# Optimization experiments

Hardware: AMD Instinct MI355X
Metric: run time of the kernel (lower is better)

The kernel has to match this reference:

```python
import jax, jax.numpy as jnp
import numpy as np

D_MODEL = 768
NUM_HEADS = 12
HEAD_DIM = D_MODEL // NUM_HEADS
THETA = 10000.0
SEQ = 4096
BATCH = 2


def setup_inputs() -> dict:
    key = jax.random.key(0)
    ks = jax.random.split(key, 5)
    std = np.sqrt(2.0 / (D_MODEL + D_MODEL)).astype(np.float32)
    x = jax.random.normal(ks[0], (BATCH, SEQ, D_MODEL), dtype=jnp.float32)
    token_positions = jnp.arange(SEQ, dtype=jnp.int32)
    # Linear stores weight as (d_out, d_in), applied as x @ W.T
    wq = jax.random.normal(ks[1], (D_MODEL, D_MODEL), dtype=jnp.float32) * std
    wk = jax.random.normal(ks[2], (D_MODEL, D_MODEL), dtype=jnp.float32) * std
    wv = jax.random.normal(ks[3], (D_MODEL, D_MODEL), dtype=jnp.float32) * std
    wo = jax.random.normal(ks[4], (D_MODEL, D_MODEL), dtype=jnp.float32) * std
    return {"x": x, "token_positions": token_positions,
            "wq": wq, "wk": wk, "wv": wv, "wo": wo}


def _apply_rope(t, positions):
    # t: [B, H, S, hd], positions: [S]
    half = HEAD_DIM // 2
    inv_freq = THETA ** (-jnp.arange(0, HEAD_DIM, 2, dtype=jnp.float32) / HEAD_DIM)  # [half]
    angles = positions.astype(jnp.float32)[:, None] * inv_freq  # [S, half]
    cos = jnp.repeat(jnp.cos(angles), 2, axis=-1)  # [S, hd]
    sin = jnp.repeat(jnp.sin(angles), 2, axis=-1)  # [S, hd]
    # rotate pairs: (-x1, x0, -x3, x2, ...)
    t2 = jnp.stack([-t[..., 1::2], t[..., ::2]], axis=-1).reshape(t.shape)
    return t * cos + t2 * sin


def reference(x, token_positions, wq, wk, wv, wo):
    B, S, D = x.shape
    H, hd = NUM_HEADS, HEAD_DIM
    q = (x @ wq.T).reshape(B, S, H, hd).transpose(0, 2, 1, 3)  # [B,H,S,hd]
    k = (x @ wk.T).reshape(B, S, H, hd).transpose(0, 2, 1, 3)
    v = (x @ wv.T).reshape(B, S, H, hd).transpose(0, 2, 1, 3)
    q = _apply_rope(q, token_positions)
    k = _apply_rope(k, token_positions)
    scale = hd ** -0.5
    scores = jnp.einsum('bhqd,bhkd->bhqk', q, k) * scale  # [B,H,S,S]
    causal = jnp.tril(jnp.ones((S, S), dtype=bool))
    scores = jnp.where(causal, scores, -jnp.inf)
    att = jax.nn.softmax(scores, axis=-1)
    out = jnp.einsum('bhqk,bhkd->bhqd', att, v)  # [B,H,S,hd]
    out = out.transpose(0, 2, 1, 3).reshape(B, S, D)
    return out @ wo.T
```

## Files before the change

kernel.cpp:

```cpp
#include <hip/hip_runtime.h>
#include <hip/hip_bf16.h>
#include <stdint.h>

#define D_MODEL 768
#define NHEADS 12
#define HD 64
#define SEQ 4096
#define BATCH 2
#define MTOT (BATCH*SEQ)
#define BHN (BATCH*NHEADS)

typedef __attribute__((ext_vector_type(8))) short short8;
typedef __attribute__((ext_vector_type(4))) float f32x4;
typedef __attribute__((ext_vector_type(16))) float f32x16;
typedef __attribute__((ext_vector_type(4))) int i32x4;

__device__ inline unsigned short f2bf(float f) {
  union { float f; unsigned u; } v; v.f = f;
  unsigned r = (v.u + 0x7FFFu + ((v.u >> 16) & 1u)) >> 16;
  return (unsigned short)r;
}
__device__ inline unsigned cvtpk_bf16(float lo, float hi) {
  unsigned r;
  asm("v_cvt_pk_bf16_f32 %0, %1, %2" : "=v"(r) : "v"(lo), "v"(hi));
  return r;
}
__device__ inline void perm32swap(unsigned &a, unsigned &b) {
  asm("v_permlane32_swap_b32 %0, %1" : "+v"(a), "+v"(b));
}
__device__ inline float exp2fast(float x) {
  float r;
  asm("v_exp_f32 %0, %1" : "=v"(r) : "v"(x));
  return r;
}
__device__ inline void gload16(const void* g, void* l) {
  __builtin_amdgcn_global_load_lds(
      (const __attribute__((address_space(1))) unsigned int*)g,
      (__attribute__((address_space(3))) unsigned int*)l, 16, 0, 0);
}

__global__ void k_conv(const float* __restrict__ x,  const float* __restrict__ wq,
                       const float* __restrict__ wk, const float* __restrict__ wv,
                       const float* __restrict__ wo,
                       unsigned short* __restrict__ xb,  unsigned short* __restrict__ wqb,
                       unsigned short* __restrict__ wkb, unsigned short* __restrict__ wvb,
                       unsigned short* __restrict__ wob)
{
  int i = blockIdx.x * blockDim.x + threadIdx.x;
  const int X4 = MTOT*D_MODEL/4;
  const int W4 = D_MODEL*D_MODEL/4;
  const float* src; unsigned short* dst; int idx;
  if (i < X4) { src = x; dst = xb; idx = i; }
  else {
    int j = i - X4;
    if      (j <   W4) { src = wq; dst = wqb; idx = j; }
    else if (j < 2*W4) { src = wk; dst = wkb; idx = j -   W4; }
    else if (j < 3*W4) { src = wv; dst = wvb; idx = j - 2*W4; }
    else if (j < 4*W4) { src = wo; dst = wob; idx = j - 3*W4; }
    else return;
  }
  float4 v = ((const float4*)src)[idx];
  ushort4 o;
  o.x = f2bf(v.x); o.y = f2bf(v.y); o.z = f2bf(v.z); o.w = f2bf(v.w);
  ((ushort4*)dst)[idx] = o;
}

__global__ void k_ropetab(const int* __restrict__ pos, float* __restrict__ ct, float* __restrict__ st) {
  int i = blockIdx.x * blockDim.x + threadIdx.x;
  if (i >= SEQ*32) return;
  int s = i >> 5, j = i & 31;
  float p = (float)pos[s];
  const float L = 0.2878231366242557f;
  float freq = __expf(-L * (float)j);
  float a = p * freq;
  ct[i] = cosf(a);
  st[i] = sinf(a);
}

__global__ __launch_bounds__(256)
void k_gemm_qkv(const unsigned short* __restrict__ X,
                const unsigned short* __restrict__ Wq,
                const unsigned short* __restrict__ Wk,
                const unsigned short* __restrict__ Wv,
                unsigned short* __restrict__ Qp,
                unsigned short* __restrict__ Kp,
                unsigned short* __restrict__ VT,
                const float* __restrict__ ct,
                const float* __restrict__ st)
{
  __shared__ __align__(16) unsigned short As[2][128*32];
  __shared__ __align__(16) unsigned short Bs[2][128*32];
  const int tid = threadIdx.x;
  const int wave = tid >> 6, lane = tid & 63;
  const int lr = lane & 15, lg = lane >> 4;
  const int wr = wave >> 1, wc = wave & 1;
  const int m0 = blockIdx.x * 128;
  const int n0 = blockIdx.y * 128;
  const int z  = blockIdx.z;
  const unsigned short* B = (z == 0) ? Wq : (z == 1) ? Wk : Wv;
  const int K = 768;

  f32x4 acc[4][4] = {};
  const int srow = tid >> 2, scol = (tid & 3) << 3;
  const unsigned short* ag = X + (size_t)(m0 + srow) * K + scol;
  const unsigned short* bg = B + (size_t)(n0 + srow) * K + scol;

  {
    char* a0 = (char*)As[0] + wave*1024;
    char* a1 = (char*)As[0] + 4096 + wave*1024;
    char* b0 = (char*)Bs[0] + wave*1024;
    char* b1 = (char*)Bs[0] + 4096 + wave*1024;
    gload16(ag, a0);
    gload16(ag + (size_t)64*K, a1);
    gload16(bg, b0);
    gload16(bg + (size_t)64*K, b1);
  }
  int cur = 0;
  for (int k0 = 0; k0 < K; k0 += 32) {
    __syncthreads();
    if (k0 + 32 < K) {
      char* a0 = (char*)As[cur^1] + wave*1024;
      char* a1 = (char*)As[cur^1] + 4096 + wave*1024;
      char* b0 = (char*)Bs[cur^1] + wave*1024;
      char* b1 = (char*)Bs[cur^1] + 4096 + wave*1024;
      gload16(ag + k0 + 32, a0);
      gload16(ag + (size_t)64*K + k0 + 32, a1);
      gload16(bg + k0 + 32, b0);
      gload16(bg + (size_t)64*K + k0 + 32, b1);
    }
    short8 af[4], bfr[4];
    #pragma unroll
    for (int i = 0; i < 4; ++i)
      af[i] = *(const short8*)&As[cur][(wr*64 + i*16 + lr)*32 + lg*8];
    #pragma unroll
    for (int j = 0; j < 4; ++j)
      bfr[j] = *(const short8*)&Bs[cur][(wc*64 + j*16 + lr)*32 + lg*8];
    #pragma unroll
    for (int i = 0; i < 4; ++i)
      #pragma unroll
      for (int j = 0; j < 4; ++j)
        acc[i][j] = __builtin_amdgcn_mfma_f32_16x16x32_bf16(af[i], bfr[j], acc[i][j], 0, 0, 0);
    cur ^= 1;
  }

  #pragma unroll
  for (int i = 0; i < 4; ++i)
    #pragma unroll
    for (int j = 0; j < 4; ++j) {
      const int n = n0 + wc*64 + j*16 + lr;
      const int h = n >> 6, d = n & (HD-1);
      if (z == 2) {
        #pragma unroll
        for (int r = 0; r < 4; ++r) {
          int m = m0 + wr*64 + i*16 + lg*4 + r;
          int bb = m >> 12, s = m & (SEQ-1);
          VT[(((size_t)bb*NHEADS + h)*HD + d)*SEQ + s] = f2bf(acc[i][j][r]);
        }
      } else {
        unsigned short* dst = (z == 0) ? Qp : Kp;
        const float* cb = ct + (d >> 1);
        const float* sb = st + (d >> 1);
        #pragma unroll
        for (int r = 0; r < 4; ++r) {
          int m = m0 + wr*64 + i*16 + lg*4 + r;
          int bb = m >> 12, s = m & (SEQ-1);
          float vv = acc[i][j][r];
          float pp = __shfl_xor(vv, 1);
          float cs = cb[s << 5], sn = sb[s << 5];
          float res = (d & 1) ? (vv*cs + pp*sn) : (vv*cs - pp*sn);
          if (z == 0) res *= 0.18033688011112043f;
          dst[(((size_t)bb*NHEADS + h)*SEQ + s)*HD + d] = f2bf(res);
        }
      }
    }
}

__global__ __launch_bounds__(256)
void k_gemm_wo(const unsigned short* __restrict__ X,
               const unsigned short* __restrict__ W,
               float* __restrict__ out)
{
  __shared__ __align__(16) unsigned short As[2][128*32];
  __shared__ __align__(16) unsigned short Bs[2][128*32];
  const int tid = threadIdx.x;
  const int wave = tid >> 6, lane = tid & 63;
  const int lr = lane & 15, lg = lane >> 4;
  const int wr = wave >> 1, wc = wave & 1;
  const int m0 = blockIdx.x * 128;
  const int n0 = blockIdx.y * 128;
  const int K = 768;

  f32x4 acc[4][4] = {};
  const int srow = tid >> 2, scol = (tid & 3) << 3;
  const unsigned short* ag = X + (size_t)(m0 + srow) * K + scol;
  const unsigned short* bg = W + (size_t)(n0 + srow) * K + scol;

  {
    char* a0 = (char*)As[0] + wave*1024;
    char* a1 = (char*)As[0] + 4096 + wave*1024;
    char* b0 = (char*)Bs[0] + wave*1024;
    char* b1 = (char*)Bs[0] + 4096 + wave*1024;
    gload16(ag, a0);
    gload16(ag + (size_t)64*K, a1);
    gload16(bg, b0);
    gload16(bg + (size_t)64*K, b1);
  }
  int cur = 0;
  for (int k0 = 0; k0 < K; k0 += 32) {
    __syncthreads();
    if (k0 + 32 < K) {
      char* a0 = (char*)As[cur^1] + wave*1024;
      char* a1 = (char*)As[cur^1] + 4096 + wave*1024;
      char* b0 = (char*)Bs[cur^1] + wave*1024;
      char* b1 = (char*)Bs[cur^1] + 4096 + wave*1024;
      gload16(ag + k0 + 32, a0);
      gload16(ag + (size_t)64*K + k0 + 32, a1);
      gload16(bg + k0 + 32, b0);
      gload16(bg + (size_t)64*K + k0 + 32, b1);
    }
    short8 af[4], bfr[4];
    #pragma unroll
    for (int i = 0; i < 4; ++i)
      af[i] = *(const short8*)&As[cur][(wr*64 + i*16 + lr)*32 + lg*8];
    #pragma unroll
    for (int j = 0; j < 4; ++j)
      bfr[j] = *(const short8*)&Bs[cur][(wc*64 + j*16 + lr)*32 + lg*8];
    #pragma unroll
    for (int i = 0; i < 4; ++i)
      #pragma unroll
      for (int j = 0; j < 4; ++j)
        acc[i][j] = __builtin_amdgcn_mfma_f32_16x16x32_bf16(af[i], bfr[j], acc[i][j], 0, 0, 0);
    cur ^= 1;
  }

  #pragma unroll
  for (int i = 0; i < 4; ++i)
    #pragma unroll
    for (int j = 0; j < 4; ++j)
      #pragma unroll
      for (int r = 0; r < 4; ++r) {
        int m = m0 + wr*64 + i*16 + lg*4 + r;
        int n = n0 + wc*64 + j*16 + lr;
        out[(size_t)m*D_MODEL + n] = acc[i][j][r];
      }
}

__global__ __launch_bounds__(256, 3)
void k_attn(const unsigned short* __restrict__ Qp,
            const unsigned short* __restrict__ Kp,
            const unsigned short* __restrict__ VT,
            unsigned short* __restrict__ AO)
{
  __shared__ __align__(16) unsigned short Ks[2][64*64];
  __shared__ __align__(16) unsigned short Vs[2][64*64];

  const int tid = threadIdx.x;
  const int wave = tid >> 6, lane = tid & 63;
  const int qcol = lane & 31, hi = lane >> 5;

  const int u = blockIdx.x;
  const int kk = u >> 8, g = u & 255;
  const int rank = (kk == 0) ? g : (kk == 1) ? (767 - g) : (256 + g);
  const int cpair = rank / 24;
  const int bh = rank - cpair * 24;

  const int b = bh / NHEADS, h = bh % NHEADS;
  const int chunk = (wave < 2) ? cpair : 63 - cpair;
  const int qw = chunk * 64 + (wave & 1) * 32;
  const int nt = 64 - cpair;
  const int myNt = qw / 64 + 1;

  const unsigned short* Qh = Qp + (size_t)bh * SEQ * HD;
  const unsigned short* Kh = Kp + (size_t)bh * SEQ * HD;
  const unsigned short* Vh = VT + (size_t)bh * HD * SEQ;

  short8 qf[4];
  #pragma unroll
  for (int ds = 0; ds < 4; ++ds)
    qf[ds] = *(const short8*)(Qh + (size_t)(qw + qcol)*HD + ds*16 + hi*8);

  f32x16 o[2] = {};
  f32x16 lv = {};

  const int g_row = tid >> 3;
  const int sgp = ((tid & 7) ^ (g_row & 7)) * 8;

  {
    char* kb0 = (char*)Ks[0] + wave*1024;
    char* kb1 = (char*)Ks[0] + 4096 + wave*1024;
    char* vb0 = (char*)Vs[0] + wave*1024;
    char* vb1 = (char*)Vs[0] + 4096 + wave*1024;
    gload16(Kh + (size_t)g_row*HD + sgp, kb0);
    gload16(Kh + (size_t)(g_row + 32)*HD + sgp, kb1);
    gload16(Vh + (size_t)g_row*SEQ + sgp, vb0);
    gload16(Vh + (size_t)(g_row + 32)*SEQ + sgp, vb1);
  }
  __syncthreads();

  int cur = 0;
  for (int kt = 0; kt < nt; ++kt) {
    if (kt + 1 < nt) {
      const size_t kb = (size_t)(kt + 1) * 64;
      char* kb0 = (char*)Ks[cur^1] + wave*1024;
      char* kb1 = (char*)Ks[cur^1] + 4096 + wave*1024;
      char* vb0 = (char*)Vs[cur^1] + wave*1024;
      char* vb1 = (char*)Vs[cur^1] + 4096 + wave*1024;
      gload16(Kh + (kb + g_row)*HD + sgp, kb0);
      gload16(Kh + (kb + g_row + 32)*HD + sgp, kb1);
      gload16(Vh + (size_t)g_row*SEQ + kb + sgp, vb0);
      gload16(Vh + (size_t)(g_row + 32)*SEQ + kb + sgp, vb1);
    }
    if (kt < myNt) {
      const char* Kb = (const char*)Ks[cur];
      const char* Vb = (const char*)Vs[cur];
      f32x16 c[2];
      __builtin_amdgcn_s_setprio(1);
      #pragma unroll
      for (int kc = 0; kc < 2; ++kc) {
        f32x16 acc = {};
        #pragma unroll
        for (int ds = 0; ds < 4; ++ds) {
          const int row = kc*32 + qcol;
          short8 kf = *(const short8*)(Kb + row*128 + ((ds*32 + hi*16) ^ ((row & 7) << 4)));
          acc = __builtin_amdgcn_mfma_f32_32x32x16_bf16(kf, qf[ds], acc, 0, 0, 0);
        }
        c[kc] = acc;
      }
      __builtin_amdgcn_s_setprio(0);
      if (kt == myNt - 1) {
        const int q = qw + qcol;
        #pragma unroll
        for (int kc = 0; kc < 2; ++kc)
          #pragma unroll
          for (int r = 0; r < 16; ++r) {
            int key = kt*64 + kc*32 + (r & 3) + 8*(r >> 2) + 4*hi;
            if (key > q) c[kc][r] = -1e30f;
          }
      }
      #pragma unroll
      for (int kc = 0; kc < 2; ++kc)
        #pragma unroll
        for (int r = 0; r < 16; ++r)
          c[kc][r] = exp2fast(c[kc][r]);
      #pragma unroll
      for (int r = 0; r < 16; ++r) lv[r] += c[0][r] + c[1][r];
      unsigned U[8][2];
      #pragma unroll
      for (int g2 = 0; g2 < 8; ++g2) {
        const int fc = g2 >> 2, gq = g2 & 3;
        U[g2][0] = cvtpk_bf16(c[fc][4*gq + 0], c[fc][4*gq + 1]);
        U[g2][1] = cvtpk_bf16(c[fc][4*gq + 2], c[fc][4*gq + 3]);
      }
      #pragma unroll
      for (int ks = 0; ks < 4; ++ks) {
        unsigned j0 = U[2*ks][0], j2 = U[2*ks+1][0];
        perm32swap(j0, j2);
        unsigned j1 = U[2*ks][1], j3 = U[2*ks+1][1];
        perm32swap(j1, j3);
        union { unsigned u[4]; short8 s; } pf;
        pf.u[0] = j0; pf.u[1] = j1; pf.u[2] = j2; pf.u[3] = j3;
        __builtin_amdgcn_s_setprio(1);
        #pragma unroll
        for (int dc = 0; dc < 2; ++dc) {
          const int row = dc*32 + qcol;
          short8 vf = *(const short8*)(Vb + row*128 + ((ks*32 + hi*16) ^ ((row & 7) << 4)));
          o[dc] = __builtin_amdgcn_mfma_f32_32x32x16_bf16(vf, pf.s, o[dc], 0, 0, 0);
        }
        __builtin_amdgcn_s_setprio(0);
      }
    }
    __syncthreads();
    cur ^= 1;
  }

  float s0 = (lv[0]+lv[1]) + (lv[2]+lv[3]);
  float s1 = (lv[4]+lv[5]) + (lv[6]+lv[7]);
  float s2 = (lv[8]+lv[9]) + (lv[10]+lv[11]);
  float s3 = (lv[12]+lv[13]) + (lv[14]+lv[15]);
  float ssum = (s0+s1) + (s2+s3);
  ssum += __shfl_xor(ssum, 32);
  const float inv = 1.0f / ssum;
  const size_t rowbase = ((size_t)b*SEQ + qw + qcol) * D_MODEL + h*HD;
  #pragma unroll
  for (int dc = 0; dc < 2; ++dc)
    #pragma unroll
    for (int g2 = 0; g2 < 4; ++g2) {
      ushort4 pk;
      pk.x = f2bf(o[dc][4*g2 + 0] * inv);
      pk.y = f2bf(o[dc][4*g2 + 1] * inv);
      pk.z = f2bf(o[dc][4*g2 + 2] * inv);
      pk.w = f2bf(o[dc][4*g2 + 3] * inv);
      const int d0 = dc*32 + 8*g2 + 4*hi;
      *(ushort4*)(AO + rowbase + d0) = pk;
    }
}

extern "C" void kernel_launch(void* const* d_in, const int* in_sizes, int n_in,
                              void* d_out, int out_size, void* d_ws, size_t ws_size,
                              hipStream_t stream)
{
  const float* x  = (const float*)d_in[0];
  const int* posi = (const int*)d_in[1];
  const float* wq = (const float*)d_in[2];
  const float* wk = (const float*)d_in[3];
  const float* wv = (const float*)d_in[4];
  const float* wo = (const float*)d_in[5];
  float* out = (float*)d_out;

  char* ws = (char*)d_ws;
  size_t off = 0;
  auto alloc = [&](size_t bytes) {
    char* p = ws + off;
    off += (bytes + 255) & ~(size_t)255;
    return p;
  };
  unsigned short* xb  = (unsigned short*)alloc((size_t)MTOT*D_MODEL*2);
  unsigned short* wqb = (unsigned short*)alloc((size_t)D_MODEL*D_MODEL*2);
  unsigned short* wkb = (unsigned short*)alloc((size_t)D_MODEL*D_MODEL*2);
  unsigned short* wvb = (unsigned short*)alloc((size_t)D_MODEL*D_MODEL*2);
  unsigned short* wob = (unsigned short*)alloc((size_t)D_MODEL*D_MODEL*2);
  unsigned short* Qb  = (unsigned short*)alloc((size_t)BHN*SEQ*HD*2);
  unsigned short* Kb  = (unsigned short*)alloc((size_t)BHN*SEQ*HD*2);
  unsigned short* VTb = (unsigned short*)alloc((size_t)BHN*HD*SEQ*2);
  unsigned short* AOb = (unsigned short*)alloc((size_t)MTOT*D_MODEL*2);
  float* ct = (float*)alloc((size_t)SEQ*32*4);
  float* st = (float*)alloc((size_t)SEQ*32*4);

  const int total4 = MTOT*D_MODEL/4 + 4*(D_MODEL*D_MODEL/4);
  k_conv<<<(total4 + 255)/256, 256, 0, stream>>>(x, wq, wk, wv, wo, xb, wqb, wkb, wvb, wob);
  k_ropetab<<<(SEQ*32 + 255)/256, 256, 0, stream>>>(posi, ct, st);

  k_gemm_qkv<<<dim3(MTOT/128, D_MODEL/128, 3), 256, 0, stream>>>(xb, wqb, wkb, wvb, Qb, Kb, VTb, ct, st);
  k_attn<<<dim3(768), 256, 0, stream>>>(Qb, Kb, VTb, AOb);
  k_gemm_wo<<<dim3(MTOT/128, D_MODEL/128), 256, 0, stream>>>(AOb, wob, out);
}
```

Measured before the change: 167.4 us.

## Triple-buffer attention K/V tiles and software-pipeline QK^T ahead of softmax

The attention kernel moves from two shared-memory K/V buffers to three, prefetching two tiles ahead, and computes the QK^T MFMAs for the next tile while the current tile's exp and PV work is still in flight. The loop is unrolled by two so the score registers can ping-pong. The RoPE cos/sin table is also transposed to [freq][seq], so the QKV epilogue can load four consecutive positions as one vector. The costs are more LDS per block, which may reduce occupancy under launch_bounds(256,3), and higher register pressure from holding two score tiles at once.

```diff
diff --git a/kernel.cpp b/kernel.cpp
--- a/kernel.cpp
+++ b/kernel.cpp
@@ -68,7 +68,7 @@
 __global__ void k_ropetab(const int* __restrict__ pos, float* __restrict__ ct, float* __restrict__ st) {
   int i = blockIdx.x * blockDim.x + threadIdx.x;
   if (i >= SEQ*32) return;
-  int s = i >> 5, j = i & 31;
+  int s = i & (SEQ-1), j = i >> 12;
   float p = (float)pos[s];
   const float L = 0.2878231366242557f;
   float freq = __expf(-L * (float)j);
@@ -158,18 +158,19 @@
         }
       } else {
         unsigned short* dst = (z == 0) ? Qp : Kp;
-        const float* cb = ct + (d >> 1);
-        const float* sb = st + (d >> 1);
+        const int jrow = d >> 1;
+        const int mb = m0 + wr*64 + i*16 + lg*4;
+        const int bb = mb >> 12;
+        const int sbase = mb & (SEQ-1);
+        f32x4 cs4 = *(const f32x4*)(ct + (size_t)jrow*SEQ + sbase);
+        f32x4 sn4 = *(const f32x4*)(st + (size_t)jrow*SEQ + sbase);
         #pragma unroll
         for (int r = 0; r < 4; ++r) {
-          int m = m0 + wr*64 + i*16 + lg*4 + r;
-          int bb = m >> 12, s = m & (SEQ-1);
           float vv = acc[i][j][r];
           float pp = __shfl_xor(vv, 1);
-          float cs = cb[s << 5], sn = sb[s << 5];
-          float res = (d & 1) ? (vv*cs + pp*sn) : (vv*cs - pp*sn);
+          float res = (d & 1) ? (vv*cs4[r] + pp*sn4[r]) : (vv*cs4[r] - pp*sn4[r]);
           if (z == 0) res *= 0.18033688011112043f;
-          dst[(((size_t)bb*NHEADS + h)*SEQ + s)*HD + d] = f2bf(res);
+          dst[(((size_t)bb*NHEADS + h)*SEQ + (sbase + r))*HD + d] = f2bf(res);
         }
       }
     }
@@ -251,8 +252,8 @@
             const unsigned short* __restrict__ VT,
             unsigned short* __restrict__ AO)
 {
-  __shared__ __align__(16) unsigned short Ks[2][64*64];
-  __shared__ __align__(16) unsigned short Vs[2][64*64];
+  __shared__ __align__(16) unsigned short Ks[3][64*64];
+  __shared__ __align__(16) unsigned short Vs[3][64*64];
 
   const int tid = threadIdx.x;
   const int wave = tid >> 6, lane = tid & 63;
@@ -285,48 +286,40 @@
   const int g_row = tid >> 3;
   const int sgp = ((tid & 7) ^ (g_row & 7)) * 8;
 
-  {
-    char* kb0 = (char*)Ks[0] + wave*1024;
-    char* kb1 = (char*)Ks[0] + 4096 + wave*1024;
-    char* vb0 = (char*)Vs[0] + wave*1024;
-    char* vb1 = (char*)Vs[0] + 4096 + wave*1024;
-    gload16(Kh + (size_t)g_row*HD + sgp, kb0);
-    gload16(Kh + (size_t)(g_row + 32)*HD + sgp, kb1);
-    gload16(Vh + (size_t)g_row*SEQ + sgp, vb0);
-    gload16(Vh + (size_t)(g_row + 32)*SEQ + sgp, vb1);
-  }
+  auto STAGE = [&](int t, int bi) {
+    const size_t kb = (size_t)t * 64;
+    gload16(Kh + (kb + g_row)*HD + sgp,        (char*)Ks[bi] + wave*1024);
+    gload16(Kh + (kb + g_row + 32)*HD + sgp,   (char*)Ks[bi] + 4096 + wave*1024);
+    gload16(Vh + (size_t)g_row*SEQ + kb + sgp,      (char*)Vs[bi] + wave*1024);
+    gload16(Vh + (size_t)(g_row + 32)*SEQ + kb + sgp, (char*)Vs[bi] + 4096 + wave*1024);
+  };
+  auto QKT = [&](int bi, f32x16 (&cc)[2]) {
+    const char* Kb = (const char*)Ks[bi];
+    __builtin_amdgcn_s_setprio(1);
+    #pragma unroll
+    for (int kc = 0; kc < 2; ++kc) {
+      f32x16 acc = {};
+      #pragma unroll
+      for (int ds = 0; ds < 4; ++ds) {
+        const int row = kc*32 + qcol;
+        short8 kf = *(const short8*)(Kb + row*128 + ((ds*32 + hi*16) ^ ((row & 7) << 4)));
+        acc = __builtin_amdgcn_mfma_f32_32x32x16_bf16(kf, qf[ds], acc, 0, 0, 0);
+      }
+      cc[kc] = acc;
+    }
+    __builtin_amdgcn_s_setprio(0);
+  };
+
+  STAGE(0, 0);
+  if (nt > 1) STAGE(1, 1);
   __syncthreads();
-
-  int cur = 0;
-  for (int kt = 0; kt < nt; ++kt) {
-    if (kt + 1 < nt) {
-      const size_t kb = (size_t)(kt + 1) * 64;
-      char* kb0 = (char*)Ks[cur^1] + wave*1024;
-      char* kb1 = (char*)Ks[cur^1] + 4096 + wave*1024;
-      char* vb0 = (char*)Vs[cur^1] + wave*1024;
-      char* vb1 = (char*)Vs[cur^1] + 4096 + wave*1024;
-      gload16(Kh + (kb + g_row)*HD + sgp, kb0);
-      gload16(Kh + (kb + g_row + 32)*HD + sgp, kb1);
-      gload16(Vh + (size_t)g_row*SEQ + kb + sgp, vb0);
-      gload16(Vh + (size_t)(g_row + 32)*SEQ + kb + sgp, vb1);
-    }
+  f32x16 cA[2], cB[2];
+  QKT(0, cA);
+
+  int kt = 0, bc = 0, bn = 1, bs = 2;
+  auto ITER = [&](f32x16 (&ccur)[2], f32x16 (&cnxt)[2]) {
+    if (kt + 2 < nt) STAGE(kt + 2, bs);
     if (kt < myNt) {
-      const char* Kb = (const char*)Ks[cur];
-      const char* Vb = (const char*)Vs[cur];
-      f32x16 c[2];
-      __builtin_amdgcn_s_setprio(1);
-      #pragma unroll
-      for (int kc = 0; kc < 2; ++kc) {
-        f32x16 acc = {};
-        #pragma unroll
-        for (int ds = 0; ds < 4; ++ds) {
-          const int row = kc*32 + qcol;
-          short8 kf = *(const short8*)(Kb + row*128 + ((ds*32 + hi*16) ^ ((row & 7) << 4)));
-          acc = __builtin_amdgcn_mfma_f32_32x32x16_bf16(kf, qf[ds], acc, 0, 0, 0);
-        }
-        c[kc] = acc;
-      }
-      __builtin_amdgcn_s_setprio(0);
       if (kt == myNt - 1) {
         const int q = qw + qcol;
         #pragma unroll
@@ -334,23 +327,25 @@
           #pragma unroll
           for (int r = 0; r < 16; ++r) {
             int key = kt*64 + kc*32 + (r & 3) + 8*(r >> 2) + 4*hi;
-            if (key > q) c[kc][r] = -1e30f;
+            if (key > q) ccur[kc][r] = -1e30f;
           }
       }
       #pragma unroll
       for (int kc = 0; kc < 2; ++kc)
         #pragma unroll
         for (int r = 0; r < 16; ++r)
-          c[kc][r] = exp2fast(c[kc][r]);
-      #pragma unroll
-      for (int r = 0; r < 16; ++r) lv[r] += c[0][r] + c[1][r];
+          ccur[kc][r] = exp2fast(ccur[kc][r]);
+      #pragma unroll
+      for (int r = 0; r < 16; ++r) lv[r] += ccur[0][r] + ccur[1][r];
+      if (kt + 1 < myNt) QKT(bn, cnxt);
       unsigned U[8][2];
       #pragma unroll
       for (int g2 = 0; g2 < 8; ++g2) {
         const int fc = g2 >> 2, gq = g2 & 3;
-        U[g2][0] = cvtpk_bf16(c[fc][4*gq + 0], c[fc][4*gq + 1]);
-        U[g2][1] = cvtpk_bf16(c[fc][4*gq + 2], c[fc][4*gq + 3]);
-      }
+        U[g2][0] = cvtpk_bf16(ccur[fc][4*gq + 0], ccur[fc][4*gq + 1]);
+        U[g2][1] = cvtpk_bf16(ccur[fc][4*gq + 2], ccur[fc][4*gq + 3]);
+      }
+      const char* Vb = (const char*)Vs[bc];
       #pragma unroll
       for (int ks = 0; ks < 4; ++ks) {
         unsigned j0 = U[2*ks][0], j2 = U[2*ks+1][0];
@@ -370,8 +365,12 @@
       }
     }
     __syncthreads();
-    cur ^= 1;
-  }
+    const int t = bc; bc = bn; bn = bs; bs = t;
+    ++kt;
+  };
+
+  while (kt + 1 < nt) { ITER(cA, cB); ITER(cB, cA); }
+  if (kt < nt) ITER(cA, cB);
 
   float s0 = (lv[0]+lv[1]) + (lv[2]+lv[3]);
   float s1 = (lv[4]+lv[5]) + (lv[6]+lv[7]);
```

Result: slower. 180.1 us (+7.6%).

## Transpose RoPE table for vector loads; compute softmax row sums via MFMA

Applied to the files above, without the earlier changes.

The RoPE cos/sin tables are now stored frequency-major, so the QK GEMM epilogue reads four consecutive positions with one vector load instead of four strided scalar loads. In the attention kernel, the per-row sum of exponentials is now produced by an extra MFMA against a vector of bf16 ones. This replaces the 32 VALU adds per tile and the final cross-lane reduction. The sum is now taken over the bf16-rounded probabilities, which matches what multiplies V, at the cost of one extra MFMA per k-step.

```diff
diff --git a/kernel.cpp b/kernel.cpp
--- a/kernel.cpp
+++ b/kernel.cpp
@@ -68,7 +68,7 @@
 __global__ void k_ropetab(const int* __restrict__ pos, float* __restrict__ ct, float* __restrict__ st) {
   int i = blockIdx.x * blockDim.x + threadIdx.x;
   if (i >= SEQ*32) return;
-  int s = i >> 5, j = i & 31;
+  int s = i & (SEQ-1), j = i >> 12;
   float p = (float)pos[s];
   const float L = 0.2878231366242557f;
   float freq = __expf(-L * (float)j);
@@ -158,18 +158,19 @@
         }
       } else {
         unsigned short* dst = (z == 0) ? Qp : Kp;
-        const float* cb = ct + (d >> 1);
-        const float* sb = st + (d >> 1);
+        const int jrow = d >> 1;
+        const int mb = m0 + wr*64 + i*16 + lg*4;
+        const int bb = mb >> 12;
+        const int sbase = mb & (SEQ-1);
+        f32x4 cs4 = *(const f32x4*)(ct + (size_t)jrow*SEQ + sbase);
+        f32x4 sn4 = *(const f32x4*)(st + (size_t)jrow*SEQ + sbase);
         #pragma unroll
         for (int r = 0; r < 4; ++r) {
-          int m = m0 + wr*64 + i*16 + lg*4 + r;
-          int bb = m >> 12, s = m & (SEQ-1);
           float vv = acc[i][j][r];
           float pp = __shfl_xor(vv, 1);
-          float cs = cb[s << 5], sn = sb[s << 5];
-          float res = (d & 1) ? (vv*cs + pp*sn) : (vv*cs - pp*sn);
+          float res = (d & 1) ? (vv*cs4[r] + pp*sn4[r]) : (vv*cs4[r] - pp*sn4[r]);
           if (z == 0) res *= 0.18033688011112043f;
-          dst[(((size_t)bb*NHEADS + h)*SEQ + s)*HD + d] = f2bf(res);
+          dst[(((size_t)bb*NHEADS + h)*SEQ + (sbase + r))*HD + d] = f2bf(res);
         }
       }
     }
@@ -279,21 +280,21 @@
   for (int ds = 0; ds < 4; ++ds)
     qf[ds] = *(const short8*)(Qh + (size_t)(qw + qcol)*HD + ds*16 + hi*8);
 
+  short8 onesf;
+  #pragma unroll
+  for (int i = 0; i < 8; ++i) onesf[i] = (short)0x3F80;
+
   f32x16 o[2] = {};
-  f32x16 lv = {};
+  f32x16 lacc = {};
 
   const int g_row = tid >> 3;
   const int sgp = ((tid & 7) ^ (g_row & 7)) * 8;
 
   {
-    char* kb0 = (char*)Ks[0] + wave*1024;
-    char* kb1 = (char*)Ks[0] + 4096 + wave*1024;
-    char* vb0 = (char*)Vs[0] + wave*1024;
-    char* vb1 = (char*)Vs[0] + 4096 + wave*1024;
-    gload16(Kh + (size_t)g_row*HD + sgp, kb0);
-    gload16(Kh + (size_t)(g_row + 32)*HD + sgp, kb1);
-    gload16(Vh + (size_t)g_row*SEQ + sgp, vb0);
-    gload16(Vh + (size_t)(g_row + 32)*SEQ + sgp, vb1);
+    gload16(Kh + (size_t)g_row*HD + sgp,          (char*)Ks[0] + wave*1024);
+    gload16(Kh + (size_t)(g_row + 32)*HD + sgp,   (char*)Ks[0] + 4096 + wave*1024);
+    gload16(Vh + (size_t)g_row*SEQ + sgp,         (char*)Vs[0] + wave*1024);
+    gload16(Vh + (size_t)(g_row + 32)*SEQ + sgp,  (char*)Vs[0] + 4096 + wave*1024);
   }
   __syncthreads();
 
@@ -301,14 +302,10 @@
   for (int kt = 0; kt < nt; ++kt) {
     if (kt + 1 < nt) {
       const size_t kb = (size_t)(kt + 1) * 64;
-      char* kb0 = (char*)Ks[cur^1] + wave*1024;
-      char* kb1 = (char*)Ks[cur^1] + 4096 + wave*1024;
-      char* vb0 = (char*)Vs[cur^1] + wave*1024;
-      char* vb1 = (char*)Vs[cur^1] + 4096 + wave*1024;
-      gload16(Kh + (kb + g_row)*HD + sgp, kb0);
-      gload16(Kh + (kb + g_row + 32)*HD + sgp, kb1);
-      gload16(Vh + (size_t)g_row*SEQ + kb + sgp, vb0);
-      gload16(Vh + (size_t)(g_row + 32)*SEQ + kb + sgp, vb1);
+      gload16(Kh + (kb + g_row)*HD + sgp,            (char*)Ks[cur^1] + wave*1024);
+      gload16(Kh + (kb + g_row + 32)*HD + sgp,       (char*)Ks[cur^1] + 4096 + wave*1024);
+      gload16(Vh + (size_t)g_row*SEQ + kb + sgp,     (char*)Vs[cur^1] + wave*1024);
+      gload16(Vh + (size_t)(g_row + 32)*SEQ + kb + sgp, (char*)Vs[cur^1] + 4096 + wave*1024);
     }
     if (kt < myNt) {
       const char* Kb = (const char*)Ks[cur];
@@ -342,8 +339,6 @@
         #pragma unroll
         for (int r = 0; r < 16; ++r)
           c[kc][r] = exp2fast(c[kc][r]);
-      #pragma unroll
-      for (int r = 0; r < 16; ++r) lv[r] += c[0][r] + c[1][r];
       unsigned U[8][2];
       #pragma unroll
       for (int g2 = 0; g2 < 8; ++g2) {
@@ -366,6 +361,7 @@
           short8 vf = *(const short8*)(Vb + row*128 + ((ks*32 + hi*16) ^ ((row & 7) << 4)));
           o[dc] = __builtin_amdgcn_mfma_f32_32x32x16_bf16(vf, pf.s, o[dc], 0, 0, 0);
         }
+        lacc = __builtin_amdgcn_mfma_f32_32x32x16_bf16(onesf, pf.s, lacc, 0, 0, 0);
         __builtin_amdgcn_s_setprio(0);
       }
     }
@@ -373,13 +369,7 @@
     cur ^= 1;
   }
 
-  float s0 = (lv[0]+lv[1]) + (lv[2]+lv[3]);
-  float s1 = (lv[4]+lv[5]) + (lv[6]+lv[7]);
-  float s2 = (lv[8]+lv[9]) + (lv[10]+lv[11]);
-  float s3 = (lv[12]+lv[13]) + (lv[14]+lv[15]);
-  float ssum = (s0+s1) + (s2+s3);
-  ssum += __shfl_xor(ssum, 32);
-  const float inv = 1.0f / ssum;
+  const float inv = 1.0f / lacc[0];
   const size_t rowbase = ((size_t)b*SEQ + qw + qcol) * D_MODEL + h*HD;
   #pragma unroll
   for (int dc = 0; dc < 2; ++dc)
```

Result: no change. 167.9 us (median of 2 runs) (+0.3%).
